# Optimization experiments

Measured on AMD Instinct MI355X. Metric: run time of the kernel, lower is better.

Reference implementation:

```python
import jax, jax.numpy as jnp
import numpy as np

NEG_SLOPE = 0.2


def _gat(x, W, a_src, a_dst, bias, src, dst, nonself, N):
    # PyG GATConv (eval mode): h = x @ W -> [N,H,C]; per-edge scores with
    # LeakyReLU, softmax over incoming edges per target node (self loops
    # re-added after removing any existing ones), weighted scatter-add.
    H, C = a_src.shape
    h = (x @ W).reshape(N, H, C)
    al_s = jnp.einsum('nhc,hc->nh', h, a_src)  # [N,H]
    al_d = jnp.einsum('nhc,hc->nh', h, a_dst)
    e = jax.nn.leaky_relu(al_s[src] + al_d[dst], NEG_SLOPE)  # [E,H]
    e = jnp.where(nonself[:, None], e, -jnp.inf)  # drop input self loops
    e_self = jax.nn.leaky_relu(al_s + al_d, NEG_SLOPE)  # added self loops [N,H]
    m = jnp.maximum(jax.ops.segment_max(e, dst, num_segments=N), e_self)
    w = jnp.exp(e - m[dst])  # masked edges -> 0
    w_self = jnp.exp(e_self - m)
    num = jax.ops.segment_sum(w[:, :, None] * h[src], dst, num_segments=N)
    num = num + w_self[:, :, None] * h
    den = jax.ops.segment_sum(w, dst, num_segments=N) + w_self
    return (num / den[:, :, None]).reshape(N, H * C) + bias


def setup_inputs() -> dict:
    N, E = 100000, 3200000
    key = jax.random.key(0)
    ks = jax.random.split(key, 20)
    s = 0.1
    return {
        'x1': jax.random.normal(ks[0], (N, 7), jnp.float32),
        'x2': jax.random.normal(ks[1], (N, 1), jnp.float32),
        'edge_index': jax.random.randint(ks[2], (2, E), 0, N, jnp.int64)
            if jax.config.jax_enable_x64 else jax.random.randint(ks[2], (2, E), 0, N, jnp.int32),
        'num_nodes': N,
        'lin1_w': s * jax.random.normal(ks[3], (1, 7), jnp.float32),
        'lin1_b': s * jax.random.normal(ks[4], (1,), jnp.float32),
        'lin2_w': s * jax.random.normal(ks[5], (1, 8), jnp.float32),
        'W1': s * jax.random.normal(ks[6], (1, 32), jnp.float32),
        'a_src1': s * jax.random.normal(ks[7], (8, 4), jnp.float32),
        'a_dst1': s * jax.random.normal(ks[8], (8, 4), jnp.float32),
        'b1': s * jax.random.normal(ks[9], (32,), jnp.float32),
        'W2': s * jax.random.normal(ks[10], (32, 16), jnp.float32),
        'a_src2': s * jax.random.normal(ks[11], (4, 4), jnp.float32),
        'a_dst2': s * jax.random.normal(ks[12], (4, 4), jnp.float32),
        'b2': s * jax.random.normal(ks[13], (16,), jnp.float32),
        'W3': s * jax.random.normal(ks[14], (16, 8), jnp.float32),
        'a_src3': s * jax.random.normal(ks[15], (2, 4), jnp.float32),
        'a_dst3': s * jax.random.normal(ks[16], (2, 4), jnp.float32),
        'b3': s * jax.random.normal(ks[17], (8,), jnp.float32),
    }


def reference(x1, x2, edge_index, num_nodes, lin1_w, lin1_b, lin2_w,
              W1, a_src1, a_dst1, b1, W2, a_src2, a_dst2, b2,
              W3, a_src3, a_dst3, b3):
    N = num_nodes
    src, dst = edge_index[0], edge_index[1]
    nonself = src != dst
    # init score + 3 GAT layers (dropouts inactive in eval mode)
    h0 = jax.nn.relu(x1 @ lin1_w.T + lin1_b)  # [N,1]
    x3 = jax.nn.relu(_gat(h0, W1, a_src1, a_dst1, b1, src, dst, nonself, N))
    x4 = jax.nn.relu(_gat(x3, W2, a_src2, a_dst2, b2, src, dst, nonself, N))
    x6 = jax.nn.relu(_gat(x4, W3, a_src3, a_dst3, b3, src, dst, nonself, N))  # [N,8]
    # Row-normalized adjacency with diagonal filled to 1 (sparse form of the
    # original dense Adj): Adj[i,j] = 1/deg[i] on edges (i!=j) and diagonal.
    ns = nonself.astype(x6.dtype)
    deg = 1.0 + jax.ops.segment_sum(ns, src, num_segments=N)  # [N]
    # local score: rowsum(Adj * (x6 x6^T))
    dots = jnp.sum(x6[src] * x6[dst], axis=-1) * ns  # [E]
    local = (jax.ops.segment_sum(dots, src, num_segments=N)
             + jnp.sum(x6 * x6, axis=-1)) / deg  # [N]
    # global score: lin2(Adj @ x6)
    R3 = (jax.ops.segment_sum(x6[dst] * ns[:, None], src, num_segments=N)
          + x6) / deg[:, None]  # [N,8]
    return local[:, None] + R3 @ lin2_w.T  # [N,1]
```

## Files before the change

### kernel.cpp

```cpp
#include <hip/hip_runtime.h>
#include <hip/hip_fp16.h>
#include <math.h>

static constexpr float NEG_SLOPE = 0.2f;
static constexpr int P      = 256;
static constexpr int CAP    = 14000;
static constexpr int CHSZ   = 4096;

__device__ __forceinline__ float lrelu(float x) { return x > 0.0f ? x : NEG_SLOPE * x; }

__device__ __forceinline__ void dm(int x, unsigned int mg, int npr, int& r, int& lk) {
    r = (int)__umulhi((unsigned int)x, mg);
    lk = x - r * npr;
    if (lk >= npr) { lk -= npr; ++r; }
    else if (lk < 0) { lk += npr; --r; }
}

union H8 { int4 i4; __half2 h2[4]; };

__device__ __forceinline__ void h8_to_f(int4 v, float* o) {
    H8 u; u.i4 = v;
#pragma unroll
    for (int k = 0; k < 4; ++k) {
        float2 f = __half22float2(u.h2[k]);
        o[2 * k] = f.x; o[2 * k + 1] = f.y;
    }
}

__device__ __forceinline__ int4 f_to_h8(const float* s) {
    H8 u;
#pragma unroll
    for (int k = 0; k < 4; ++k)
        u.h2[k] = __float22half2_rn(make_float2(s[2 * k], s[2 * k + 1]));
    return u.i4;
}

__global__ __launch_bounds__(256) void part2_kernel(
    const int* __restrict__ src, const int* __restrict__ dst,
    int* __restrict__ gcount,
    unsigned int* __restrict__ stgd, unsigned int* __restrict__ stgs,
    int E, int npr, unsigned int mg)
{
    __shared__ int cntw[4 * P];
    __shared__ int base[P];
    __shared__ int pref[P];
    __shared__ int wsum[4];
    __shared__ unsigned int buf[CHSZ];
    __shared__ unsigned char rid[CHSZ];
    const int dir = blockIdx.x & 1;
    const int c = blockIdx.x >> 1;
    const int i0 = c * CHSZ;
    const int i1 = min(i0 + CHSZ, E);
    const int tot = i1 - i0;
    const int tid = threadIdx.x;
    const int lane = tid & 63, w = tid >> 6;
    const int* key = dir ? (src + i0) : (dst + i0);
    const int* val = dir ? (dst + i0) : (src + i0);
    unsigned int* stg = dir ? stgs : stgd;
    int* gc = gcount + dir * P;
    int* mycnt = cntw + w * P;
#pragma unroll
    for (int q = 0; q < 4; ++q) cntw[q * P + tid] = 0;
    __syncthreads();
    const int nv = tot >> 2;
    const int4* k4 = (const int4*)key;
    for (int t = tid; t < nv; t += 256) {
        int4 k = k4[t];
        int r, lk;
        dm(k.x, mg, npr, r, lk); atomicAdd(&mycnt[r], 1);
        dm(k.y, mg, npr, r, lk); atomicAdd(&mycnt[r], 1);
        dm(k.z, mg, npr, r, lk); atomicAdd(&mycnt[r], 1);
        dm(k.w, mg, npr, r, lk); atomicAdd(&mycnt[r], 1);
    }
    for (int i = (nv << 2) + tid; i < tot; i += 256) {
        int r, lk;
        dm(key[i], mg, npr, r, lk);
        atomicAdd(&mycnt[r], 1);
    }
    __syncthreads();
    int c0 = cntw[0 * P + tid], c1 = cntw[1 * P + tid];
    int c2 = cntw[2 * P + tid], c3 = cntw[3 * P + tid];
    int tb = c0 + c1 + c2 + c3;
    base[tid] = atomicAdd(&gc[tid], tb);
    int x = tb;
#pragma unroll
    for (int off = 1; off < 64; off <<= 1) {
        int y = __shfl_up(x, off);
        if (lane >= off) x += y;
    }
    if (lane == 63) wsum[w] = x;
    __syncthreads();
    int wpref = 0;
#pragma unroll
    for (int k = 0; k < 4; ++k) if (k < w) wpref += wsum[k];
    int ex = x + wpref - tb;
    pref[tid] = ex;
    cntw[0 * P + tid] = ex;
    cntw[1 * P + tid] = ex + c0;
    cntw[2 * P + tid] = ex + c0 + c1;
    cntw[3 * P + tid] = ex + c0 + c1 + c2;
    __syncthreads();
    int* mytick = cntw + w * P;
    for (int t = tid; t < nv; t += 256) {
        int4 k = k4[t];
        const int4* v4 = (const int4*)val;
        int4 v = v4[t];
        int r, lk, p;
        dm(k.x, mg, npr, r, lk); p = atomicAdd(&mytick[r], 1);
        buf[p] = ((unsigned int)lk << 17) | (unsigned int)v.x; rid[p] = (unsigned char)r;
        dm(k.y, mg, npr, r, lk); p = atomicAdd(&mytick[r], 1);
        buf[p] = ((unsigned int)lk << 17) | (unsigned int)v.y; rid[p] = (unsigned char)r;
        dm(k.z, mg, npr, r, lk); p = atomicAdd(&mytick[r], 1);
        buf[p] = ((unsigned int)lk << 17) | (unsigned int)v.z; rid[p] = (unsigned char)r;
        dm(k.w, mg, npr, r, lk); p = atomicAdd(&mytick[r], 1);
        buf[p] = ((unsigned int)lk << 17) | (unsigned int)v.w; rid[p] = (unsigned char)r;
    }
    for (int i = (nv << 2) + tid; i < tot; i += 256) {
        int r, lk;
        dm(key[i], mg, npr, r, lk);
        int p = atomicAdd(&mytick[r], 1);
        buf[p] = ((unsigned int)lk << 17) | (unsigned int)val[i];
        rid[p] = (unsigned char)r;
    }
    __syncthreads();
    for (int i = tid; i < tot; i += 256) {
        int r = (int)rid[i];
        int b = base[r] + (i - pref[r]);
        if (b < CAP) stg[(size_t)r * CAP + b] = buf[i];
    }
}

__global__ __launch_bounds__(512) void ebase_kernel(
    const int* __restrict__ gtot, int* __restrict__ ebase)
{
    __shared__ int sm[2 * P];
    int tid = threadIdx.x;
    int v = gtot[tid];
    sm[tid] = v;
    __syncthreads();
#pragma unroll
    for (int off = 1; off < P; off <<= 1) {
        int t = ((tid & (P - 1)) >= off) ? sm[tid - off] : 0;
        __syncthreads();
        sm[tid] += t;
        __syncthreads();
    }
    ebase[tid] = sm[tid] - v;
}

__global__ __launch_bounds__(512) void build_kernel(
    const unsigned int* __restrict__ stgd, const unsigned int* __restrict__ stgs,
    const int* __restrict__ gtot, const int* __restrict__ ebase,
    int* __restrict__ col_dst, int* __restrict__ col_src,
    int* __restrict__ deg_dst, int* __restrict__ deg_src,
    int* __restrict__ row_dst, int* __restrict__ row_src,
    int N, int npr)
{
    __shared__ int cntw[2 * 512];
    __shared__ int scn[512];
    __shared__ int outv[CAP];
    const int dir = blockIdx.x >> 8;
    const int r = blockIdx.x & (P - 1);
    const unsigned int* stg = (dir ? stgs : stgd) + (size_t)r * CAP;
    int tot = gtot[dir * P + r];
    if (tot > CAP) tot = CAP;
    const int n0 = r * npr;
    const int nb = min(npr, N - n0);
    const int tid = threadIdx.x;
    const int g = tid >> 8;
    int* mycnt = cntw + g * 512;
    cntw[tid] = 0; cntw[512 + tid] = 0;
    __syncthreads();
    for (int i = tid; i < tot; i += 512)
        atomicAdd(&mycnt[stg[i] >> 17], 1);
    __syncthreads();
    int c0 = cntw[tid], c1 = cntw[512 + tid];
    int v = c0 + c1;
    scn[tid] = v;
    __syncthreads();
#pragma unroll
    for (int off = 1; off < 512; off <<= 1) {
        int t = (tid >= off) ? scn[tid - off] : 0;
        __syncthreads();
        scn[tid] += t;
        __syncthreads();
    }
    int ex = scn[tid] - v;
    const int eb = ebase[dir * P + r];
    if (tid < nb) {
        (dir ? deg_src : deg_dst)[n0 + tid] = v;
        (dir ? row_src : row_dst)[n0 + tid] = eb + ex;
    }
    cntw[tid] = ex;
    cntw[512 + tid] = ex + c0;
    __syncthreads();
    for (int i = tid; i < tot; i += 512) {
        unsigned int w = stg[i];
        int t = atomicAdd(&mycnt[w >> 17], 1);
        outv[t] = (int)(w & 0x1FFFFu);
    }
    __syncthreads();
    int* col = (dir ? col_src : col_dst) + eb;
    for (int i = tid; i < tot; i += 512) col[i] = outv[i];
}

__global__ __launch_bounds__(256) void l1h0_kernel(
    const float* __restrict__ x1, const float* __restrict__ lin1_w,
    const float* __restrict__ lin1_b, float* __restrict__ h0, int N)
{
    int n = blockIdx.x * blockDim.x + threadIdx.x;
    if (n >= N) return;
    float acc = lin1_b[0];
#pragma unroll
    for (int k = 0; k < 7; ++k) acc = fmaf(x1[n * 7 + k], lin1_w[k], acc);
    h0[n] = fmaxf(acc, 0.0f);
}

__global__ __launch_bounds__(256) void gat_gather1_kernel(
    const int* __restrict__ row_start, const int* __restrict__ degv,
    const int* __restrict__ col, const float* __restrict__ h0,
    const float* __restrict__ W1, const float* __restrict__ a_src,
    const float* __restrict__ a_dst, const float* __restrict__ bias,
    float* __restrict__ x3, int N)
{
    int t = blockIdx.x * 256 + threadIdx.x;
    int n = t >> 3, lane = t & 7;
    if (n >= N) return;
    float cs[8], cd[8];
#pragma unroll
    for (int hd = 0; hd < 8; ++hd) {
        float s = 0.0f, d = 0.0f;
#pragma unroll
        for (int c = 0; c < 4; ++c) {
            s = fmaf(W1[hd * 4 + c], a_src[hd * 4 + c], s);
            d = fmaf(W1[hd * 4 + c], a_dst[hd * 4 + c], d);
        }
        cs[hd] = s; cd[hd] = d;
    }
    float h0n = h0[n];
    float wh[8], den[8], adn[8];
#pragma unroll
    for (int hd = 0; hd < 8; ++hd) {
        adn[hd] = h0n * cd[hd];
        if (lane == 0) {
            float w = __expf(lrelu(h0n * cs[hd] + adn[hd]));
            den[hd] = w; wh[hd] = w * h0n;
        } else { den[hd] = 0.0f; wh[hd] = 0.0f; }
    }
    int start = row_start[n];
    int end = start + degv[n];
    for (int e = start + lane; e < end; e += 8) {
        int s = col[e];
        if (s == n) continue;
        float hs = h0[s];
#pragma unroll
        for (int hd = 0; hd < 8; ++hd) {
            float w = __expf(lrelu(hs * cs[hd] + adn[hd]));
            den[hd] += w;
            wh[hd] = fmaf(w, hs, wh[hd]);
        }
    }
#pragma unroll
    for (int m = 1; m < 8; m <<= 1) {
#pragma unroll
        for (int hd = 0; hd < 8; ++hd) {
            den[hd] += __shfl_xor(den[hd], m);
            wh[hd]  += __shfl_xor(wh[hd], m);
        }
    }
    float fct = wh[lane] / den[lane];
    const float4 wv = ((const float4*)W1)[lane];
    const float4 bb = ((const float4*)bias)[lane];
    float4 r;
    r.x = fmaxf(fmaf(fct, wv.x, bb.x), 0.0f);
    r.y = fmaxf(fmaf(fct, wv.y, bb.y), 0.0f);
    r.z = fmaxf(fmaf(fct, wv.z, bb.z), 0.0f);
    r.w = fmaxf(fmaf(fct, wv.w, bb.w), 0.0f);
    ((float4*)x3)[(size_t)n * 8 + lane] = r;
}

template <int IN, int HC>
__global__ __launch_bounds__(256) void gat_node_f16_kernel(
    const float* __restrict__ x, const float* __restrict__ W,
    int4* __restrict__ hp, int N)
{
    int n = blockIdx.x * blockDim.x + threadIdx.x;
    if (n >= N) return;
    float xv[IN];
#pragma unroll
    for (int k = 0; k < IN; ++k) xv[k] = x[n * IN + k];
    float hv[HC];
#pragma unroll
    for (int j = 0; j < HC; ++j) {
        float acc = 0.0f;
#pragma unroll
        for (int k = 0; k < IN; ++k) acc = fmaf(xv[k], W[k * HC + j], acc);
        hv[j] = acc;
    }
#pragma unroll
    for (int q = 0; q < HC / 8; ++q)
        hp[(size_t)n * (HC / 8) + q] = f_to_h8(hv + q * 8);
}

__global__ __launch_bounds__(256) void gat_gather2_kernel(
    const int* __restrict__ row_start, const int* __restrict__ degv,
    const int* __restrict__ col, const int4* __restrict__ hp,
    const float* __restrict__ a_src, const float* __restrict__ a_dst,
    const float* __restrict__ bias, float* __restrict__ xout, int N)
{
    int t = blockIdx.x * 256 + threadIdx.x;
    int n = t >> 3, lane = t & 7;
    if (n >= N) return;
    float As[16], Ad[16];
#pragma unroll
    for (int j = 0; j < 16; ++j) { As[j] = a_src[j]; Ad[j] = a_dst[j]; }
    float hn[16];
    h8_to_f(hp[(size_t)n * 2], hn);
    h8_to_f(hp[(size_t)n * 2 + 1], hn + 8);
    float ald[4];
#pragma unroll
    for (int hd = 0; hd < 4; ++hd) {
        float d = 0.0f;
#pragma unroll
        for (int c = 0; c < 4; ++c) d = fmaf(hn[hd * 4 + c], Ad[hd * 4 + c], d);
        ald[hd] = d;
    }
    float num[16], den[4];
    if (lane == 0) {
#pragma unroll
        for (int hd = 0; hd < 4; ++hd) {
            float a = 0.0f;
#pragma unroll
            for (int c = 0; c < 4; ++c) a = fmaf(hn[hd * 4 + c], As[hd * 4 + c], a);
            float w = __expf(lrelu(a + ald[hd]));
            den[hd] = w;
#pragma unroll
            for (int c = 0; c < 4; ++c) num[hd * 4 + c] = w * hn[hd * 4 + c];
        }
    } else {
#pragma unroll
        for (int j = 0; j < 16; ++j) num[j] = 0.0f;
#pragma unroll
        for (int hd = 0; hd < 4; ++hd) den[hd] = 0.0f;
    }
    int start = row_start[n];
    int end = start + degv[n];
    for (int e = start + lane; e < end; e += 8) {
        int s = col[e];
        if (s == n) continue;
        float hs[16];
        h8_to_f(hp[(size_t)s * 2], hs);
        h8_to_f(hp[(size_t)s * 2 + 1], hs + 8);
#pragma unroll
        for (int hd = 0; hd < 4; ++hd) {
            float a = 0.0f;
#pragma unroll
            for (int c = 0; c < 4; ++c) a = fmaf(hs[hd * 4 + c], As[hd * 4 + c], a);
            float w = __expf(lrelu(a + ald[hd]));
            den[hd] += w;
#pragma unroll
            for (int c = 0; c < 4; ++c) num[hd * 4 + c] = fmaf(w, hs[hd * 4 + c], num[hd * 4 + c]);
        }
    }
#pragma unroll
    for (int m = 1; m < 8; m <<= 1) {
#pragma unroll
        for (int hd = 0; hd < 4; ++hd) den[hd] += __shfl_xor(den[hd], m);
#pragma unroll
        for (int j = 0; j < 16; ++j) num[j] += __shfl_xor(num[j], m);
    }
    if (lane < 4) {
        float inv = 1.0f / den[lane];
        const float4 bb = ((const float4*)bias)[lane];
        float4 r;
        r.x = fmaxf(fmaf(num[lane * 4 + 0], inv, bb.x), 0.0f);
        r.y = fmaxf(fmaf(num[lane * 4 + 1], inv, bb.y), 0.0f);
        r.z = fmaxf(fmaf(num[lane * 4 + 2], inv, bb.z), 0.0f);
        r.w = fmaxf(fmaf(num[lane * 4 + 3], inv, bb.w), 0.0f);
        ((float4*)xout)[(size_t)n * 4 + lane] = r;
    }
}

__global__ __launch_bounds__(256) void gat_gather3_kernel(
    const int* __restrict__ row_start, const int* __restrict__ degv,
    const int* __restrict__ col, const int4* __restrict__ hp,
    const float* __restrict__ a_src, const float* __restrict__ a_dst,
    const float* __restrict__ bias, int4* __restrict__ x6p, int N)
{
    int t = blockIdx.x * 256 + threadIdx.x;
    int n = t >> 2, lane = t & 3;
    if (n >= N) return;
    float As[8], Ad[8];
#pragma unroll
    for (int j = 0; j < 8; ++j) { As[j] = a_src[j]; Ad[j] = a_dst[j]; }
    float hn[8];
    h8_to_f(hp[n], hn);
    float ald[2];
#pragma unroll
    for (int hd = 0; hd < 2; ++hd) {
        float d = 0.0f;
#pragma unroll
        for (int c = 0; c < 4; ++c) d = fmaf(hn[hd * 4 + c], Ad[hd * 4 + c], d);
        ald[hd] = d;
    }
    float num[8], den[2];
    if (lane == 0) {
#pragma unroll
        for (int hd = 0; hd < 2; ++hd) {
            float a = 0.0f;
#pragma unroll
            for (int c = 0; c < 4; ++c) a = fmaf(hn[hd * 4 + c], As[hd * 4 + c], a);
            float w = __expf(lrelu(a + ald[hd]));
            den[hd] = w;
#pragma unroll
            for (int c = 0; c < 4; ++c) num[hd * 4 + c] = w * hn[hd * 4 + c];
        }
    } else {
#pragma unroll
        for (int j = 0; j < 8; ++j) num[j] = 0.0f;
        den[0] = den[1] = 0.0f;
    }
    int start = row_start[n];
    int end = start + degv[n];
    for (int e = start + lane; e < end; e += 4) {
        int s = col[e];
        if (s == n) continue;
        float hs[8];
        h8_to_f(hp[s], hs);
#pragma unroll
        for (int hd = 0; hd < 2; ++hd) {
            float a = 0.0f;
#pragma unroll
            for (int c = 0; c < 4; ++c) a = fmaf(hs[hd * 4 + c], As[hd * 4 + c], a);
            float w = __expf(lrelu(a + ald[hd]));
            den[hd] += w;
#pragma unroll
            for (int c = 0; c < 4; ++c) num[hd * 4 + c] = fmaf(w, hs[hd * 4 + c], num[hd * 4 + c]);
        }
    }
#pragma unroll
    for (int m = 1; m < 4; m <<= 1) {
        den[0] += __shfl_xor(den[0], m);
        den[1] += __shfl_xor(den[1], m);
#pragma unroll
        for (int j = 0; j < 8; ++j) num[j] += __shfl_xor(num[j], m);
    }
    if (lane == 0) {
        float o[8];
        float i0 = 1.0f / den[0], i1 = 1.0f / den[1];
#pragma unroll
        for (int c = 0; c < 4; ++c) {
            o[c]     = fmaxf(fmaf(num[c], i0, bias[c]), 0.0f);
            o[4 + c] = fmaxf(fmaf(num[4 + c], i1, bias[4 + c]), 0.0f);
        }
        x6p[n] = f_to_h8(o);
    }
}

__global__ __launch_bounds__(256) void score_gather_kernel(
    const int* __restrict__ row_start, const int* __restrict__ degv,
    const int* __restrict__ col, const int4* __restrict__ x6p,
    const float* __restrict__ lin2_w, float* __restrict__ out, int N)
{
    int t = blockIdx.x * 256 + threadIdx.x;
    int n = t >> 2, lane = t & 3;
    if (n >= N) return;
    float sx[8];
    h8_to_f(x6p[n], sx);
    float r[8];
    int sc = 0;
    if (lane == 0) {
#pragma unroll
        for (int j = 0; j < 8; ++j) r[j] = sx[j];
    } else {
#pragma unroll
        for (int j = 0; j < 8; ++j) r[j] = 0.0f;
    }
    int start = row_start[n];
    int dg = degv[n];
    int end = start + dg;
    for (int e = start + lane; e < end; e += 4) {
        int d = col[e];
        if (d == n) { ++sc; continue; }
        float dx[8];
        h8_to_f(x6p[d], dx);
#pragma unroll
        for (int j = 0; j < 8; ++j) r[j] += dx[j];
    }
#pragma unroll
    for (int m = 1; m < 4; m <<= 1) {
        sc += __shfl_xor(sc, m);
#pragma unroll
        for (int j = 0; j < 8; ++j) r[j] += __shfl_xor(r[j], m);
    }
    if (lane == 0) {
        float invd = 1.0f / (1.0f + (float)(dg - sc));
        float loc = 0.0f, g = 0.0f;
#pragma unroll
        for (int j = 0; j < 8; ++j) {
            loc = fmaf(sx[j], r[j], loc);
            g   = fmaf(r[j], lin2_w[j], g);
        }
        out[n] = (loc + g) * invd;
    }
}

extern "C" void kernel_launch(void* const* d_in, const int* in_sizes, int n_in,
                              void* d_out, int out_size, void* d_ws, size_t ws_size,
                              hipStream_t stream)
{
    const float* x1     = (const float*)d_in[0];
    const int*   ei     = (const int*)d_in[2];
    const float* lin1_w = (const float*)d_in[4];
    const float* lin1_b = (const float*)d_in[5];
    const float* lin2_w = (const float*)d_in[6];
    const float* W1     = (const float*)d_in[7];
    const float* a_src1 = (const float*)d_in[8];
    const float* a_dst1 = (const float*)d_in[9];
    const float* b1     = (const float*)d_in[10];
    const float* W2     = (const float*)d_in[11];
    const float* a_src2 = (const float*)d_in[12];
    const float* a_dst2 = (const float*)d_in[13];
    const float* b2     = (const float*)d_in[14];
    const float* W3     = (const float*)d_in[15];
    const float* a_src3 = (const float*)d_in[16];
    const float* a_dst3 = (const float*)d_in[17];
    const float* b3     = (const float*)d_in[18];
    float* out = (float*)d_out;

    const int N = in_sizes[0] / 7;
    const int E = in_sizes[2] / 2;
    const int* src = ei;
    const int* dst = ei + E;

    const int npr = (N + P - 1) / P;
    const unsigned int mg = (unsigned int)((0x100000000ULL + npr - 1) / (unsigned long long)npr);
    const int PB = (E + CHSZ - 1) / CHSZ;

    size_t Ns = (size_t)N, Es = (size_t)E;
    int* ideg_dst = (int*)d_ws;
    int* ideg_src = ideg_dst + Ns;
    int* irow_dst = ideg_src + Ns;
    int* irow_src = irow_dst + Ns;
    int* gcount   = irow_src + Ns;
    int* iebase   = gcount + 2 * P;
    int* icol_dst = iebase + 2 * P;
    int* icol_src = icol_dst + Es;
    float* f = (float*)(icol_src + Es);
    unsigned int* stgd = (unsigned int*)f;
    unsigned int* stgs = stgd + (size_t)P * CAP;
    float* h0  = f;
    float* x3  = f + Ns;
    int4*  h2p = (int4*)(f + 33 * Ns);
    float* x4  = f + 41 * Ns;
    int4*  h3p = (int4*)(f + 57 * Ns);
    int4*  x6p = (int4*)(f + 61 * Ns);

    const int TB = 256;
    const int gN = (N + TB - 1) / TB;
    const int g8 = (8 * N + TB - 1) / TB;
    const int g4 = (4 * N + TB - 1) / TB;

    hipMemsetAsync(gcount, 0, 2 * P * sizeof(int), stream);
    part2_kernel<<<2 * PB, 256, 0, stream>>>(src, dst, gcount, stgd, stgs, E, npr, mg);
    ebase_kernel<<<1, 2 * P, 0, stream>>>(gcount, iebase);
    build_kernel<<<2 * P, 512, 0, stream>>>(stgd, stgs, gcount, iebase,
                                            icol_dst, icol_src,
                                            ideg_dst, ideg_src,
                                            irow_dst, irow_src, N, npr);

    l1h0_kernel<<<gN, TB, 0, stream>>>(x1, lin1_w, lin1_b, h0, N);
    gat_gather1_kernel<<<g8, TB, 0, stream>>>(irow_dst, ideg_dst, icol_dst,
                                              h0, W1, a_src1, a_dst1, b1, x3, N);

    gat_node_f16_kernel<32, 16><<<gN, TB, 0, stream>>>(x3, W2, h2p, N);
    gat_gather2_kernel<<<g8, TB, 0, stream>>>(irow_dst, ideg_dst, icol_dst,
                                              h2p, a_src2, a_dst2, b2, x4, N);

    gat_node_f16_kernel<16, 8><<<gN, TB, 0, stream>>>(x4, W3, h3p, N);
    gat_gather3_kernel<<<g4, TB, 0, stream>>>(irow_dst, ideg_dst, icol_dst,
                                              h3p, a_src3, a_dst3, b3, x6p, N);

    score_gather_kernel<<<g4, TB, 0, stream>>>(irow_src, ideg_src, icol_src,
                                               x6p, lin2_w, out, N);
}
```

Before: 271.9 us.

## Fuse per-node GAT projections into gather epilogues and widen partition blocks

The next layer's linear projection (x@W2, x@W3 to fp16) moves into the epilogues of the layer-1 and layer-2 gather kernels. This removes two node kernels and the fp32 x3/x4 round trips through global memory. The partition kernel also grows from 256 to 512 threads with 8 per-wave count histograms, to add parallelism in the bucketing pass. The cost is redundant projection work per lane, more shuffles and registers in the gather kernels, and more shared memory in the partition kernel.

```diff
diff --git a/kernel.cpp b/kernel.cpp
--- a/kernel.cpp
+++ b/kernel.cpp
@@ -35,16 +35,16 @@
     return u.i4;
 }
 
-__global__ __launch_bounds__(256) void part2_kernel(
+__global__ __launch_bounds__(512) void part2_kernel(
     const int* __restrict__ src, const int* __restrict__ dst,
     int* __restrict__ gcount,
     unsigned int* __restrict__ stgd, unsigned int* __restrict__ stgs,
     int E, int npr, unsigned int mg)
 {
-    __shared__ int cntw[4 * P];
+    __shared__ int cntw[8 * P];
     __shared__ int base[P];
     __shared__ int pref[P];
-    __shared__ int wsum[4];
+    __shared__ int wsum[8];
     __shared__ unsigned int buf[CHSZ];
     __shared__ unsigned char rid[CHSZ];
     const int dir = blockIdx.x & 1;
@@ -59,12 +59,11 @@
     unsigned int* stg = dir ? stgs : stgd;
     int* gc = gcount + dir * P;
     int* mycnt = cntw + w * P;
-#pragma unroll
-    for (int q = 0; q < 4; ++q) cntw[q * P + tid] = 0;
+    for (int i = tid; i < 8 * P; i += 512) cntw[i] = 0;
     __syncthreads();
     const int nv = tot >> 2;
     const int4* k4 = (const int4*)key;
-    for (int t = tid; t < nv; t += 256) {
+    for (int t = tid; t < nv; t += 512) {
         int4 k = k4[t];
         int r, lk;
         dm(k.x, mg, npr, r, lk); atomicAdd(&mycnt[r], 1);
@@ -72,36 +71,40 @@
         dm(k.z, mg, npr, r, lk); atomicAdd(&mycnt[r], 1);
         dm(k.w, mg, npr, r, lk); atomicAdd(&mycnt[r], 1);
     }
-    for (int i = (nv << 2) + tid; i < tot; i += 256) {
+    for (int i = (nv << 2) + tid; i < tot; i += 512) {
         int r, lk;
         dm(key[i], mg, npr, r, lk);
         atomicAdd(&mycnt[r], 1);
     }
     __syncthreads();
-    int c0 = cntw[0 * P + tid], c1 = cntw[1 * P + tid];
-    int c2 = cntw[2 * P + tid], c3 = cntw[3 * P + tid];
-    int tb = c0 + c1 + c2 + c3;
-    base[tid] = atomicAdd(&gc[tid], tb);
-    int x = tb;
-#pragma unroll
-    for (int off = 1; off < 64; off <<= 1) {
-        int y = __shfl_up(x, off);
-        if (lane >= off) x += y;
-    }
-    if (lane == 63) wsum[w] = x;
-    __syncthreads();
-    int wpref = 0;
-#pragma unroll
-    for (int k = 0; k < 4; ++k) if (k < w) wpref += wsum[k];
-    int ex = x + wpref - tb;
-    pref[tid] = ex;
-    cntw[0 * P + tid] = ex;
-    cntw[1 * P + tid] = ex + c0;
-    cntw[2 * P + tid] = ex + c0 + c1;
-    cntw[3 * P + tid] = ex + c0 + c1 + c2;
+    int cq[8];
+    int tb = 0, x = 0;
+    if (tid < P) {
+#pragma unroll
+        for (int q = 0; q < 8; ++q) { cq[q] = cntw[q * P + tid]; tb += cq[q]; }
+        base[tid] = atomicAdd(&gc[tid], tb);
+        x = tb;
+#pragma unroll
+        for (int off = 1; off < 64; off <<= 1) {
+            int y = __shfl_up(x, off);
+            if (lane >= off) x += y;
+        }
+        if (lane == 63) wsum[w] = x;
+    }
+    __syncthreads();
+    if (tid < P) {
+        int wpref = 0;
+#pragma unroll
+        for (int k = 0; k < 4; ++k) if (k < w) wpref += wsum[k];
+        int ex = x + wpref - tb;
+        pref[tid] = ex;
+        int acc = ex;
+#pragma unroll
+        for (int q = 0; q < 8; ++q) { cntw[q * P + tid] = acc; acc += cq[q]; }
+    }
     __syncthreads();
     int* mytick = cntw + w * P;
-    for (int t = tid; t < nv; t += 256) {
+    for (int t = tid; t < nv; t += 512) {
         int4 k = k4[t];
         const int4* v4 = (const int4*)val;
         int4 v = v4[t];
@@ -115,7 +118,7 @@
         dm(k.w, mg, npr, r, lk); p = atomicAdd(&mytick[r], 1);
         buf[p] = ((unsigned int)lk << 17) | (unsigned int)v.w; rid[p] = (unsigned char)r;
     }
-    for (int i = (nv << 2) + tid; i < tot; i += 256) {
+    for (int i = (nv << 2) + tid; i < tot; i += 512) {
         int r, lk;
         dm(key[i], mg, npr, r, lk);
         int p = atomicAdd(&mytick[r], 1);
@@ -123,7 +126,7 @@
         rid[p] = (unsigned char)r;
     }
     __syncthreads();
-    for (int i = tid; i < tot; i += 256) {
+    for (int i = tid; i < tot; i += 512) {
         int r = (int)rid[i];
         int b = base[r] + (i - pref[r]);
         if (b < CAP) stg[(size_t)r * CAP + b] = buf[i];
@@ -221,7 +224,7 @@
     const int* __restrict__ col, const float* __restrict__ h0,
     const float* __restrict__ W1, const float* __restrict__ a_src,
     const float* __restrict__ a_dst, const float* __restrict__ bias,
-    float* __restrict__ x3, int N)
+    const float* __restrict__ W2, int4* __restrict__ h2p, int N)
 {
     int t = blockIdx.x * 256 + threadIdx.x;
     int n = t >> 3, lane = t & 7;
@@ -271,42 +274,35 @@
     float fct = wh[lane] / den[lane];
     const float4 wv = ((const float4*)W1)[lane];
     const float4 bb = ((const float4*)bias)[lane];
-    float4 r;
-    r.x = fmaxf(fmaf(fct, wv.x, bb.x), 0.0f);
-    r.y = fmaxf(fmaf(fct, wv.y, bb.y), 0.0f);
-    r.z = fmaxf(fmaf(fct, wv.z, bb.z), 0.0f);
-    r.w = fmaxf(fmaf(fct, wv.w, bb.w), 0.0f);
-    ((float4*)x3)[(size_t)n * 8 + lane] = r;
-}
-
-template <int IN, int HC>
-__global__ __launch_bounds__(256) void gat_node_f16_kernel(
-    const float* __restrict__ x, const float* __restrict__ W,
-    int4* __restrict__ hp, int N)
-{
-    int n = blockIdx.x * blockDim.x + threadIdx.x;
-    if (n >= N) return;
-    float xv[IN];
-#pragma unroll
-    for (int k = 0; k < IN; ++k) xv[k] = x[n * IN + k];
-    float hv[HC];
-#pragma unroll
-    for (int j = 0; j < HC; ++j) {
-        float acc = 0.0f;
-#pragma unroll
-        for (int k = 0; k < IN; ++k) acc = fmaf(xv[k], W[k * HC + j], acc);
-        hv[j] = acc;
-    }
-#pragma unroll
-    for (int q = 0; q < HC / 8; ++q)
-        hp[(size_t)n * (HC / 8) + q] = f_to_h8(hv + q * 8);
+    float xr[4];
+    xr[0] = fmaxf(fmaf(fct, wv.x, bb.x), 0.0f);
+    xr[1] = fmaxf(fmaf(fct, wv.y, bb.y), 0.0f);
+    xr[2] = fmaxf(fmaf(fct, wv.z, bb.z), 0.0f);
+    xr[3] = fmaxf(fmaf(fct, wv.w, bb.w), 0.0f);
+    float pj[16];
+#pragma unroll
+    for (int j = 0; j < 16; ++j) pj[j] = 0.0f;
+    const float* wbase = W2 + lane * 64;
+#pragma unroll
+    for (int c2 = 0; c2 < 4; ++c2) {
+#pragma unroll
+        for (int j = 0; j < 16; ++j)
+            pj[j] = fmaf(xr[c2], wbase[c2 * 16 + j], pj[j]);
+    }
+#pragma unroll
+    for (int m = 1; m < 8; m <<= 1) {
+#pragma unroll
+        for (int j = 0; j < 16; ++j) pj[j] += __shfl_xor(pj[j], m);
+    }
+    if (lane < 2) h2p[(size_t)n * 2 + lane] = f_to_h8(pj + lane * 8);
 }
 
 __global__ __launch_bounds__(256) void gat_gather2_kernel(
     const int* __restrict__ row_start, const int* __restrict__ degv,
     const int* __restrict__ col, const int4* __restrict__ hp,
     const float* __restrict__ a_src, const float* __restrict__ a_dst,
-    const float* __restrict__ bias, float* __restrict__ xout, int N)
+    const float* __restrict__ bias, const float* __restrict__ W3,
+    int4* __restrict__ h3p, int N)
 {
     int t = blockIdx.x * 256 + threadIdx.x;
     int n = t >> 3, lane = t & 7;
@@ -369,16 +365,20 @@
 #pragma unroll
         for (int j = 0; j < 16; ++j) num[j] += __shfl_xor(num[j], m);
     }
-    if (lane < 4) {
-        float inv = 1.0f / den[lane];
-        const float4 bb = ((const float4*)bias)[lane];
-        float4 r;
-        r.x = fmaxf(fmaf(num[lane * 4 + 0], inv, bb.x), 0.0f);
-        r.y = fmaxf(fmaf(num[lane * 4 + 1], inv, bb.y), 0.0f);
-        r.z = fmaxf(fmaf(num[lane * 4 + 2], inv, bb.z), 0.0f);
-        r.w = fmaxf(fmaf(num[lane * 4 + 3], inv, bb.w), 0.0f);
-        ((float4*)xout)[(size_t)n * 4 + lane] = r;
-    }
+    float invd[4];
+#pragma unroll
+    for (int hd = 0; hd < 4; ++hd) invd[hd] = 1.0f / den[hd];
+    float pj[8];
+#pragma unroll
+    for (int j = 0; j < 8; ++j) pj[j] = 0.0f;
+#pragma unroll
+    for (int k = 0; k < 16; ++k) {
+        float xk = fmaxf(fmaf(num[k], invd[k >> 2], bias[k]), 0.0f);
+        const float* wrow = W3 + k * 8;
+#pragma unroll
+        for (int j = 0; j < 8; ++j) pj[j] = fmaf(xk, wrow[j], pj[j]);
+    }
+    if (lane == 0) h3p[n] = f_to_h8(pj);
 }
 
 __global__ __launch_bounds__(256) void gat_gather3_kernel(
@@ -550,11 +550,9 @@
     unsigned int* stgd = (unsigned int*)f;
     unsigned int* stgs = stgd + (size_t)P * CAP;
     float* h0  = f;
-    float* x3  = f + Ns;
-    int4*  h2p = (int4*)(f + 33 * Ns);
-    float* x4  = f + 41 * Ns;
-    int4*  h3p = (int4*)(f + 57 * Ns);
-    int4*  x6p = (int4*)(f + 61 * Ns);
+    int4*  h2p = (int4*)(f + Ns);
+    int4*  h3p = (int4*)(f + 9 * Ns);
+    int4*  x6p = (int4*)(f + 13 * Ns);
 
     const int TB = 256;
     const int gN = (N + TB - 1) / TB;
@@ -562,7 +560,7 @@
     const int g4 = (4 * N + TB - 1) / TB;
 
     hipMemsetAsync(gcount, 0, 2 * P * sizeof(int), stream);
-    part2_kernel<<<2 * PB, 256, 0, stream>>>(src, dst, gcount, stgd, stgs, E, npr, mg);
+    part2_kernel<<<2 * PB, 512, 0, stream>>>(src, dst, gcount, stgd, stgs, E, npr, mg);
     ebase_kernel<<<1, 2 * P, 0, stream>>>(gcount, iebase);
     build_kernel<<<2 * P, 512, 0, stream>>>(stgd, stgs, gcount, iebase,
                                             icol_dst, icol_src,
@@ -571,13 +569,11 @@
 
     l1h0_kernel<<<gN, TB, 0, stream>>>(x1, lin1_w, lin1_b, h0, N);
     gat_gather1_kernel<<<g8, TB, 0, stream>>>(irow_dst, ideg_dst, icol_dst,
-                                              h0, W1, a_src1, a_dst1, b1, x3, N);
-
-    gat_node_f16_kernel<32, 16><<<gN, TB, 0, stream>>>(x3, W2, h2p, N);
+                                              h0, W1, a_src1, a_dst1, b1, W2, h2p, N);
+
     gat_gather2_kernel<<<g8, TB, 0, stream>>>(irow_dst, ideg_dst, icol_dst,
-                                              h2p, a_src2, a_dst2, b2, x4, N);
-
-    gat_node_f16_kernel<16, 8><<<gN, TB, 0, stream>>>(x4, W3, h3p, N);
+                                              h2p, a_src2, a_dst2, b2, W3, h3p, N);
+
     gat_gather3_kernel<<<g4, TB, 0, stream>>>(irow_dst, ideg_dst, icol_dst,
                                               h3p, a_src3, a_dst3, b3, x6p, N);
 
```

Measured after the change: 272.6 us. About the same (+0.3%).
